# Kernel tuning notes

Hardware: AMD Instinct MI355X
Metric: run time of the kernel (lower is better)

Reference implementation:

```python
import jax, jax.numpy as jnp
import numpy as np

B, L, D = 4, 2048, 1024
H, DK, DV = 4, 256, 256
CHUNK = 32
MIN_FLOOR, MAX_FLOOR = 0.01, 0.1
EPS = 1e-5


def _l2norm(x):
    return x * jax.lax.rsqrt(jnp.sum(x * x, -1, keepdims=True) + 1e-6)


def _causal_dwconv(x, w):
    # x: [b, L, C], w: [C, k] -> depthwise causal 1d conv
    b, l, c = x.shape
    k = w.shape[-1]
    xt = jnp.transpose(x, (0, 2, 1))
    y = jax.lax.conv_general_dilated(xt, w[:, None, :], (1,), [(k - 1, 0)],
                                     dimension_numbers=('NCH', 'OIH', 'NCH'),
                                     feature_group_count=c)
    return jnp.transpose(y, (0, 2, 1))


def _delta_rule_chunkwise(q, k, v, beta, chunk=CHUNK):
    # q,k: [b,h,L,dk]; v: [b,h,L,dv]; beta: [b,h,L]; L % chunk == 0
    b, h, l, dk = q.shape
    dv = v.shape[-1]
    q = _l2norm(q)
    k = _l2norm(k)
    v = v * beta[..., None]
    kb = k * beta[..., None]
    n = l // chunk
    resh = lambda t: t.reshape(b, h, n, chunk, t.shape[-1])
    q, k, v, kb = resh(q), resh(k), resh(v), resh(kb)
    tri = jnp.triu(jnp.ones((chunk, chunk), bool))        # incl diag
    strict = jnp.triu(jnp.ones((chunk, chunk), bool), 1)  # excl diag
    att = jnp.where(tri, 0.0, -(kb @ jnp.swapaxes(k, -1, -2)))
    # UT transform: forward substitution building (I - lower)^{-1}
    for i in range(1, chunk):
        upd = jnp.einsum('bhnj,bhnjk->bhnk', att[..., i, :], att)
        att = att.at[..., i, :i].add(upd[..., :i])
    att = att + jnp.eye(chunk, dtype=att.dtype)
    u = att @ v
    w = att @ kb

    def step(S, xs):
        q_i, k_i, u_i, w_i = xs  # [b,h,chunk,d]
        local = jnp.where(strict, 0.0, q_i @ jnp.swapaxes(k_i, -1, -2))
        u_adj = u_i - w_i @ S
        o_i = q_i @ S + local @ u_adj
        return S + jnp.swapaxes(k_i, -1, -2) @ u_adj, o_i

    xs = tuple(jnp.moveaxis(t, 2, 0) for t in (q, k, u, w))
    S0 = jnp.zeros((b, h, dk, dv), q.dtype)
    S, o = jax.lax.scan(step, S0, xs)
    return jnp.moveaxis(o, 0, 2).reshape(b, h, l, dv), S


def _rmsnorm(x, w):
    return x * jax.lax.rsqrt(jnp.mean(x * x, -1, keepdims=True) + EPS) * w


def setup_inputs():
    key = jax.random.key(0)
    ks = jax.random.split(key, 16)
    s = 0.02
    return {
        'hidden_states': jax.random.normal(ks[0], (B, L, D), jnp.float32),
        'W_q': jax.random.normal(ks[1], (D, H * DK), jnp.float32) * s,
        'W_k': jax.random.normal(ks[2], (D, H * DK), jnp.float32) * s,
        'W_v': jax.random.normal(ks[3], (D, H * DV), jnp.float32) * s,
        'W_b': jax.random.normal(ks[4], (D, H), jnp.float32) * s,
        'conv_w_q': jax.random.normal(ks[5], (H * DK, 4), jnp.float32) * 0.3,
        'conv_w_k': jax.random.normal(ks[6], (H * DK, 4), jnp.float32) * 0.3,
        'conv_w_v': jax.random.normal(ks[7], (H * DV, 4), jnp.float32) * 0.3,
        'fir_short_w': jax.random.normal(ks[8], (H, DV, 3), jnp.float32) * 0.1,
        'fir_long_w': jax.random.normal(ks[9], (H, DV, 31), jnp.float32) * 0.1,
        'W_fuse1': jax.random.normal(ks[10], (D + 3 * H * DV, 2 * D), jnp.float32) * s,
        'b_fuse1': jnp.zeros((2 * D,), jnp.float32),
        'W_fuse2': jax.random.normal(ks[11], (2 * D, H * 4), jnp.float32) * s,
        'b_fuse2': jnp.zeros((H * 4,), jnp.float32).at[3::4].set(4.0),
        'others_log_tau': jnp.zeros((H,), jnp.float32),
        'norm_w': jnp.ones((DV,), jnp.float32),
        'W_o': jax.random.normal(ks[12], (H * DV, D), jnp.float32) * s,
    }


def reference(hidden_states, W_q, W_k, W_v, W_b, conv_w_q, conv_w_k, conv_w_v,
              fir_short_w, fir_long_w, W_fuse1, b_fuse1, W_fuse2, b_fuse2,
              others_log_tau, norm_w, W_o):
    b, l, d = hidden_states.shape
    # projections + mandatory short conv (silu activation)
    q = jax.nn.silu(_causal_dwconv(hidden_states @ W_q, conv_w_q))
    k = jax.nn.silu(_causal_dwconv(hidden_states @ W_k, conv_w_k))
    v = jax.nn.silu(_causal_dwconv(hidden_states @ W_v, conv_w_v))
    q = q.reshape(b, l, H, DK)
    k = k.reshape(b, l, H, DK)
    v = v.reshape(b, l, H, DV)
    beta = jax.nn.sigmoid(hidden_states @ W_b)  # [b,l,H]
    delta_out, _ = _delta_rule_chunkwise(
        jnp.transpose(q, (0, 2, 1, 3)), jnp.transpose(k, (0, 2, 1, 3)),
        jnp.transpose(v, (0, 2, 1, 3)), jnp.transpose(beta, (0, 2, 1)))
    delta_out = jnp.transpose(delta_out, (0, 2, 1, 3))  # [b,l,H,DV]
    # depthwise FIR paths on v
    vc = v.reshape(b, l, H * DV)
    fir_s = _causal_dwconv(vc, fir_short_w.reshape(H * DV, -1)).reshape(b, l, H, DV)
    fir_l = _causal_dwconv(vc, fir_long_w.reshape(H * DV, -1)).reshape(b, l, H, DV)
    # fusion gate MLP
    gate_in = jnp.concatenate([hidden_states, fir_s.reshape(b, l, -1),
                               fir_l.reshape(b, l, -1), delta_out.reshape(b, l, -1)], -1)
    hid = jax.nn.gelu(gate_in @ W_fuse1 + b_fuse1, approximate=False)
    logits = (hid @ W_fuse2 + b_fuse2).reshape(b, l, H, 4)
    p_raw = jax.nn.sigmoid(logits[..., 3])
    # token-adaptive context floor
    floor = MIN_FLOOR + (MAX_FLOOR - MIN_FLOOR) * (1.0 - p_raw)
    p_val = (1.0 - floor) * p_raw
    tau = jnp.exp(others_log_tau)  # per-head temperature
    others = jax.nn.softmax(logits[..., :3] / tau[None, None, :, None], -1)
    p_ctx = (1.0 - p_val)[..., None] * others
    o = (p_ctx[..., 0:1] * fir_s + p_ctx[..., 1:2] * fir_l +
         p_ctx[..., 2:3] * delta_out + p_val[..., None] * v)
    o = _rmsnorm(o, norm_w)
    return o.reshape(b, l, H * DV) @ W_o
```

## Files before the change

kernel.cpp:

```cpp
#include <hip/hip_runtime.h>
#include <hip/hip_bf16.h>

#define B_ 4
#define L_ 2048
#define D_ 1024
#define H_ 4
#define DK_ 256
#define DV_ 256
#define NCH 64
#define NTOK 8192

typedef __attribute__((ext_vector_type(8))) short bf16x8;
typedef __attribute__((ext_vector_type(4))) float f32x4;
typedef unsigned int u32;

__device__ __forceinline__ float bu2f(unsigned short u) {
    union { unsigned int i; float f; } x; x.i = ((unsigned int)u) << 16; return x.f;
}
__device__ __forceinline__ unsigned short f2bu(float f) {
    union { __hip_bfloat16 h; unsigned short u; } x; x.h = __float2bfloat16(f); return x.u;
}
#define MFMA16(a, b, c) __builtin_amdgcn_mfma_f32_16x16x32_bf16(a, b, c, 0, 0, 0)

__device__ __forceinline__ void gload16(const void* g, void* l) {
    __builtin_amdgcn_global_load_lds(
        (const __attribute__((address_space(1))) u32*)g,
        (__attribute__((address_space(3))) u32*)l, 16, 0, 0);
}

__global__ __launch_bounds__(256) void k_transpose(const float* __restrict__ in,
                                                   unsigned short* __restrict__ out,
                                                   int K, int N) {
    __shared__ float tile[32][33];
    int k0 = blockIdx.y * 32, n0 = blockIdx.x * 32;
    int tx = threadIdx.x & 31, ty = threadIdx.x >> 5;
#pragma unroll
    for (int r = 0; r < 4; ++r)
        tile[ty + 8 * r][tx] = in[(long)(k0 + ty + 8 * r) * N + n0 + tx];
    __syncthreads();
#pragma unroll
    for (int r = 0; r < 4; ++r)
        out[(long)(n0 + ty + 8 * r) * K + k0 + tx] = f2bu(tile[tx][ty + 8 * r]);
}

__global__ __launch_bounds__(256) void k_padT2(const float* __restrict__ W,
                                               unsigned short* __restrict__ out) {
    long idx = (long)blockIdx.x * 256 + threadIdx.x;
    int n = (int)(idx >> 11), k = (int)(idx & 2047);
    out[idx] = (n < 16) ? f2bu(W[k * 16 + n]) : (unsigned short)0;
}

__global__ __launch_bounds__(256) void k_cvt_beta(const float4* __restrict__ hs4,
                                                  const float* __restrict__ W_b,
                                                  unsigned short* __restrict__ gate_in,
                                                  float* __restrict__ beta) {
    int tok = blockIdx.x;
    int tid = threadIdx.x;
    float4 v = hs4[(long)tok * 256 + tid];
    ushort4 o;
    o.x = f2bu(v.x); o.y = f2bu(v.y); o.z = f2bu(v.z); o.w = f2bu(v.w);
    *reinterpret_cast<ushort4*>(&gate_in[(long)tok * 4096 + tid * 4]) = o;
    const float4* wb = reinterpret_cast<const float4*>(W_b);
    int c4 = tid * 4;
    float4 w0 = wb[c4], w1 = wb[c4 + 1], w2 = wb[c4 + 2], w3 = wb[c4 + 3];
    float s[4];
    s[0] = v.x * w0.x + v.y * w1.x + v.z * w2.x + v.w * w3.x;
    s[1] = v.x * w0.y + v.y * w1.y + v.z * w2.y + v.w * w3.y;
    s[2] = v.x * w0.z + v.y * w1.z + v.z * w2.z + v.w * w3.z;
    s[3] = v.x * w0.w + v.y * w1.w + v.z * w2.w + v.w * w3.w;
    int wave = tid >> 6, lane = tid & 63;
#pragma unroll
    for (int off = 32; off; off >>= 1)
#pragma unroll
        for (int h = 0; h < 4; ++h) s[h] += __shfl_down(s[h], off);
    __shared__ float red[4][4];
    if (lane == 0)
#pragma unroll
        for (int h = 0; h < 4; ++h) red[wave][h] = s[h];
    __syncthreads();
    if (tid < 4) {
        int h = tid;
        float tot = red[0][h] + red[1][h] + red[2][h] + red[3][h];
        int b = tok >> 11, l = tok & 2047;
        beta[((long)(b * H_ + h)) * L_ + l] = 1.f / (1.f + expf(-tot));
    }
}

template <int EPI>
__global__ __launch_bounds__(256, 3) void k_gemm(const unsigned short* __restrict__ A, int lda,
                                                 const unsigned short* __restrict__ BT, int ldb,
                                                 void* __restrict__ Cout, int ldc,
                                                 const float* __restrict__ bias,
                                                 int K, int gx) {
    __shared__ __align__(16) unsigned short As[128][64];
    __shared__ __align__(16) unsigned short Bs[128][64];
    const int tid = threadIdx.x;
    const int wave = tid >> 6, lane = tid & 63;
    const int wm = wave & 1, wn = wave >> 1;
    const int lr = lane & 15, lg = lane >> 4;
    const int nwg = gridDim.x;
    const int cpx = nwg >> 3;
    const int orig = blockIdx.x;
    const int wg = (orig & 7) * cpx + (orig >> 3);
    const int m0 = (wg / gx) * 128, n0 = (wg % gx) * 128;
    const int srow = wave * 32 + (lane >> 3);
    const int scol = (((lane & 7) ^ ((lane >> 3) & 7))) * 8;
    const unsigned short* Ap = &A[(long)(m0 + srow) * lda + scol];
    const unsigned short* Bp = &BT[(long)(n0 + srow) * ldb + scol];
    unsigned short* AsB = &As[wave * 32][0];
    unsigned short* BsB = &Bs[wave * 32][0];
    const unsigned short* AsF = &As[0][0];
    const unsigned short* BsF = &Bs[0][0];
    f32x4 acc[4][4] = {};
    for (int k0 = 0; k0 < K; k0 += 64) {
#pragma unroll
        for (int g = 0; g < 4; ++g) {
            gload16(Ap + (long)g * 8 * lda + k0, AsB + g * 8 * 64);
            gload16(Bp + (long)g * 8 * ldb + k0, BsB + g * 8 * 64);
        }
        __syncthreads();
#pragma unroll
        for (int ks = 0; ks < 2; ++ks) {
            bf16x8 af[4], bfr[4];
#pragma unroll
            for (int mt = 0; mt < 4; ++mt) {
                int r = wm * 64 + mt * 16 + lr;
                af[mt] = *reinterpret_cast<const bf16x8*>(
                    AsF + r * 64 + (((ks * 4 + lg) ^ (lr & 7)) * 8));
            }
#pragma unroll
            for (int nt = 0; nt < 4; ++nt) {
                int r = wn * 64 + nt * 16 + lr;
                bfr[nt] = *reinterpret_cast<const bf16x8*>(
                    BsF + r * 64 + (((ks * 4 + lg) ^ (lr & 7)) * 8));
            }
#pragma unroll
            for (int mt = 0; mt < 4; ++mt)
#pragma unroll
                for (int nt = 0; nt < 4; ++nt)
                    acc[mt][nt] = MFMA16(af[mt], bfr[nt], acc[mt][nt]);
        }
        __syncthreads();
    }
#pragma unroll
    for (int mt = 0; mt < 4; ++mt)
#pragma unroll
        for (int nt = 0; nt < 4; ++nt)
#pragma unroll
            for (int r = 0; r < 4; ++r) {
                int row = m0 + wm * 64 + mt * 16 + lg * 4 + r;
                int col = n0 + wn * 64 + nt * 16 + lr;
                float v = acc[mt][nt][r];
                if (EPI == 2) {
                    v += bias[col];
                    v = 0.5f * v * (1.f + erff(v * 0.70710678118f));
                }
                if (EPI == 0)
                    reinterpret_cast<float*>(Cout)[(long)row * ldc + col] = v;
                else
                    reinterpret_cast<unsigned short*>(Cout)[(long)row * ldc + col] = f2bu(v);
            }
}

__global__ __launch_bounds__(256) void k_fuse2(const unsigned short* __restrict__ hid,
                                               const unsigned short* __restrict__ Wf2Tp,
                                               float* __restrict__ logits4) {
    const int mt = blockIdx.x, kq = blockIdx.y;
    const int tid = threadIdx.x, wave = tid >> 6, lane = tid & 63;
    const int lr = lane & 15, lg = lane >> 4;
    const int m0 = mt * 128 + wave * 32;
    const int kb = kq * 512;
    const unsigned short* a0p = hid + (long)(m0 + lr) * 2048 + kb + lg * 8;
    const unsigned short* a1p = a0p + (long)16 * 2048;
    const unsigned short* bp = Wf2Tp + (long)lr * 2048 + kb + lg * 8;
    f32x4 acc0 = {0, 0, 0, 0}, acc1 = {0, 0, 0, 0};
#pragma unroll 4
    for (int kk = 0; kk < 16; ++kk) {
        bf16x8 a0 = *reinterpret_cast<const bf16x8*>(a0p + kk * 32);
        bf16x8 a1 = *reinterpret_cast<const bf16x8*>(a1p + kk * 32);
        bf16x8 b = *reinterpret_cast<const bf16x8*>(bp + kk * 32);
        acc0 = MFMA16(a0, b, acc0);
        acc1 = MFMA16(a1, b, acc1);
    }
    float* out = logits4 + (long)kq * NTOK * 16;
#pragma unroll
    for (int r = 0; r < 4; ++r) {
        out[(long)(m0 + lg * 4 + r) * 16 + lr] = acc0[r];
        out[(long)(m0 + 16 + lg * 4 + r) * 16 + lr] = acc1[r];
    }
}

__global__ __launch_bounds__(256) void k_conv_silu(const unsigned short* __restrict__ QKVp,
                                                   const float* __restrict__ cwq,
                                                   const float* __restrict__ cwk,
                                                   const float* __restrict__ cwv,
                                                   unsigned short* __restrict__ qn,
                                                   unsigned short* __restrict__ kn,
                                                   unsigned short* __restrict__ v_blc) {
    int tok = blockIdx.x;
    int b = tok >> 11, l = tok & 2047;
    int t = threadIdx.x;
    float y[12];
#pragma unroll
    for (int j = 0; j < 12; ++j) {
        int c = t + 256 * j;
        const float* cw = (j < 4) ? &cwq[c * 4] : (j < 8) ? &cwk[(c - 1024) * 4] : &cwv[(c - 2048) * 4];
        float s = 0.f;
#pragma unroll
        for (int jj = 0; jj < 4; ++jj) {
            int tl = l - 3 + jj;
            if (tl >= 0) s += bu2f(QKVp[((long)(b * L_ + tl)) * 3072 + c]) * cw[jj];
        }
        y[j] = s / (1.f + expf(-s));
    }
    float sq[8];
#pragma unroll
    for (int j = 0; j < 8; ++j) sq[j] = y[j] * y[j];
    int wave = t >> 6, lane = t & 63;
#pragma unroll
    for (int off = 32; off; off >>= 1)
#pragma unroll
        for (int j = 0; j < 8; ++j) sq[j] += __shfl_down(sq[j], off);
    __shared__ float red[4][8];
    if (lane == 0)
#pragma unroll
        for (int j = 0; j < 8; ++j) red[wave][j] = sq[j];
    __syncthreads();
    float tot[8];
#pragma unroll
    for (int j = 0; j < 8; ++j) tot[j] = red[0][j] + red[1][j] + red[2][j] + red[3][j];
#pragma unroll
    for (int h = 0; h < 4; ++h) {
        float sc = rsqrtf(tot[h] + 1e-6f);
        qn[((long)(b * H_ + h) * L_ + l) * 256 + t] = f2bu(y[h] * sc);
    }
#pragma unroll
    for (int h = 0; h < 4; ++h) {
        float sc = rsqrtf(tot[4 + h] + 1e-6f);
        kn[((long)(b * H_ + h) * L_ + l) * 256 + t] = f2bu(y[4 + h] * sc);
    }
#pragma unroll
    for (int h = 0; h < 4; ++h)
        v_blc[(long)tok * 1024 + h * 256 + t] = f2bu(y[8 + h]);
}

__global__ __launch_bounds__(256) void k_delta_chunk(const unsigned short* __restrict__ qn,
                                                     const unsigned short* __restrict__ kn,
                                                     const unsigned short* __restrict__ v_blc,
                                                     const float* __restrict__ beta,
                                                     unsigned short* __restrict__ u_buf,
                                                     unsigned short* __restrict__ w_buf,
                                                     unsigned short* __restrict__ local_buf,
                                                     unsigned short* __restrict__ kT_buf) {
    int bid = blockIdx.x;
    int n = bid & 63, bh = bid >> 6;
    int b = bh >> 2, h = bh & 3;
    int t0 = n * 32;
    __shared__ __align__(16) unsigned short k_s[32][264];
    __shared__ __align__(16) unsigned short vbT[256][40];
    __shared__ __align__(16) unsigned short kbT[256][40];
    __shared__ __align__(16) float att[32][33];
    __shared__ __align__(16) unsigned short att_b[32][40];
    __shared__ float bet[32];
    int tid = threadIdx.x, wave = tid >> 6, lane = tid & 63;
    int lr = lane & 15, lg = lane >> 4;

    {
        int row = tid >> 3;
        int cc = (tid & 7) * 32;
        float brow = beta[(long)bh * L_ + t0 + row];
        if ((tid & 7) == 0) bet[row] = brow;
        const uint4* kp = reinterpret_cast<const uint4*>(&kn[((long)bh * L_ + t0 + row) * 256 + cc]);
        const uint4* vp = reinterpret_cast<const uint4*>(&v_blc[((long)(b * L_ + t0 + row)) * 1024 + h * 256 + cc]);
        unsigned short kv[32], vv[32];
#pragma unroll
        for (int g = 0; g < 4; ++g) {
            uint4 x = kp[g];
            *reinterpret_cast<uint4*>(&kv[g * 8]) = x;
            *reinterpret_cast<uint4*>(&k_s[row][cc + g * 8]) = x;
            *reinterpret_cast<uint4*>(&vv[g * 8]) = vp[g];
        }
#pragma unroll
        for (int e = 0; e < 32; ++e) {
            kbT[cc + e][row] = f2bu(bu2f(kv[e]) * brow);
            vbT[cc + e][row] = f2bu(bu2f(vv[e]) * brow);
        }
    }
    __syncthreads();

    {
        unsigned short tmp[32];
#pragma unroll
        for (int t = 0; t < 32; ++t) tmp[t] = k_s[t][tid];
#pragma unroll
        for (int g = 0; g < 4; ++g)
            *reinterpret_cast<uint4*>(&kT_buf[((long)bid * 256 + tid) * 32 + g * 8]) =
                *reinterpret_cast<uint4*>(&tmp[g * 8]);
    }

    {
        int i0 = (wave & 1) * 16, j0 = (wave >> 1) * 16;
        f32x4 G = {0, 0, 0, 0}, S2 = {0, 0, 0, 0};
#pragma unroll
        for (int kk = 0; kk < 8; ++kk) {
            bf16x8 bk = *reinterpret_cast<const bf16x8*>(&k_s[j0 + lr][kk * 32 + lg * 8]);
            bf16x8 ak = *reinterpret_cast<const bf16x8*>(&k_s[i0 + lr][kk * 32 + lg * 8]);
            bf16x8 aq = *reinterpret_cast<const bf16x8*>(&qn[((long)bh * L_ + t0 + i0 + lr) * 256 + kk * 32 + lg * 8]);
            G = MFMA16(ak, bk, G);
            S2 = MFMA16(aq, bk, S2);
        }
#pragma unroll
        for (int r = 0; r < 4; ++r) {
            int i = i0 + lg * 4 + r, j = j0 + lr;
            att[i][j] = (j < i) ? -bet[i] * G[r] : 0.f;
            local_buf[(long)bid * 1024 + i * 32 + j] = f2bu((j <= i) ? S2[r] : 0.f);
        }
    }
    __syncthreads();

    for (int i = 1; i < 32; ++i) {
        float upd = 0.f;
        if (tid < i) {
            for (int j = tid + 1; j < i; ++j) upd += att[i][j] * att[j][tid];
        }
        __syncthreads();
        if (tid < i) att[i][tid] += upd;
        __syncthreads();
    }
    for (int e = tid; e < 1024; e += 256) {
        int i = e >> 5, j = e & 31;
        att_b[i][j] = f2bu(att[i][j] + ((i == j) ? 1.f : 0.f));
    }
    __syncthreads();

    {
        int mt = wave & 1;
        bf16x8 afr = *reinterpret_cast<const bf16x8*>(&att_b[mt * 16 + lr][lg * 8]);
        f32x4 z = {0, 0, 0, 0};
#pragma unroll
        for (int ntt = 0; ntt < 8; ++ntt) {
            int n0c = (wave >> 1) * 128 + ntt * 16;
            bf16x8 bu = *reinterpret_cast<const bf16x8*>(&vbT[n0c + lr][lg * 8]);
            bf16x8 bw = *reinterpret_cast<const bf16x8*>(&kbT[n0c + lr][lg * 8]);
            f32x4 ut = MFMA16(afr, bu, z);
            f32x4 wt = MFMA16(afr, bw, z);
#pragma unroll
            for (int r = 0; r < 4; ++r) {
                int t = mt * 16 + lg * 4 + r, c = n0c + lr;
                u_buf[((long)bid * 32 + t) * 256 + c] = f2bu(ut[r]);
                w_buf[((long)bid * 32 + t) * 256 + c] = f2bu(wt[r]);
            }
        }
    }
}

__global__ __launch_bounds__(256) void k_scan(const unsigned short* __restrict__ qn,
                                              const unsigned short* __restrict__ u_buf,
                                              const unsigned short* __restrict__ w_buf,
                                              const unsigned short* __restrict__ local_buf,
                                              const unsigned short* __restrict__ kT_buf,
                                              unsigned short* __restrict__ gate_in) {
    int bid = blockIdx.x;
    int bh = bid & 15, dvb = bid >> 4;
    int b = bh >> 2, h = bh & 3;
    int dc0 = dvb * 16;
    __shared__ __align__(16) unsigned short Tb[16][264];
    __shared__ __align__(16) unsigned short uaT[16][40];
    const int tid = threadIdx.x, wave = tid >> 6, lane = tid & 63;
    const int lr = lane & 15, lg = lane >> 4;
    const int wi = wave & 1;
    const bool isW = wave < 2;
    const int c0w = wave * 64;
    f32x4 Tacc[4] = {};
    for (int e = tid; e < 16 * 264; e += 256) (&Tb[0][0])[e] = 0;
    const unsigned short* q_bh = qn + (long)bh * L_ * 256;
    const unsigned short* u_bh = u_buf + (long)bh * 64 * 8192;
    const unsigned short* w_bh = w_buf + (long)bh * 64 * 8192;
    const unsigned short* l_bh = local_buf + (long)bh * 64 * 1024;
    const unsigned short* kT_bh = kT_buf + (long)bh * 64 * 8192;
    const unsigned short* wq_base = (isW ? w_bh : q_bh) + (16 * wi + lr) * 256;
    const unsigned short* u_base = u_bh + (16 * wi + lg * 4) * 256 + dc0 + lr;
    const unsigned short* l_base = l_bh + (16 * wi + lr) * 32 + lg * 8;
    const unsigned short* kT_base = kT_bh + (c0w + lr) * 32 + lg * 8;
    bf16x8 wqA[8], kB[4], lA = {};
    float uv[4];
    auto prefetch = [&](int n) {
        long o8 = (long)n * 8192;
#pragma unroll
        for (int kk = 0; kk < 8; ++kk)
            wqA[kk] = *reinterpret_cast<const bf16x8*>(wq_base + o8 + kk * 32 + lg * 8);
#pragma unroll
        for (int cc = 0; cc < 4; ++cc)
            kB[cc] = *reinterpret_cast<const bf16x8*>(kT_base + o8 + cc * 512);
        if (isW) {
#pragma unroll
            for (int r = 0; r < 4; ++r) uv[r] = bu2f(u_base[o8 + r * 256]);
        } else {
            lA = *reinterpret_cast<const bf16x8*>(l_base + (long)n * 1024);
        }
    };
    prefetch(0);
    __syncthreads();
    for (int n = 0; n < 64; ++n) {
        f32x4 P0 = {0, 0, 0, 0}, P1 = {0, 0, 0, 0};
#pragma unroll
        for (int kk = 0; kk < 8; kk += 2) {
            bf16x8 t0 = *reinterpret_cast<const bf16x8*>(&Tb[lr][kk * 32 + lg * 8]);
            bf16x8 t1 = *reinterpret_cast<const bf16x8*>(&Tb[lr][(kk + 1) * 32 + lg * 8]);
            P0 = MFMA16(wqA[kk], t0, P0);
            P1 = MFMA16(wqA[kk + 1], t1, P1);
        }
        f32x4 P;
#pragma unroll
        for (int r = 0; r < 4; ++r) P[r] = P0[r] + P1[r];
        if (isW) {
#pragma unroll
            for (int r = 0; r < 4; ++r)
                uaT[lr][16 * wi + lg * 4 + r] = f2bu(uv[r] - P[r]);
        }
        bf16x8 kBc[4];
#pragma unroll
        for (int cc = 0; cc < 4; ++cc) kBc[cc] = kB[cc];
        bf16x8 lAc = lA;
        if (n + 1 < 64) prefetch(n + 1);
        __syncthreads();
        bf16x8 uaA = *reinterpret_cast<const bf16x8*>(&uaT[lr][lg * 8]);
        if (!isW) {
            f32x4 O = MFMA16(lAc, uaA, P);
#pragma unroll
            for (int r = 0; r < 4; ++r) {
                long row = (long)b * L_ + n * 32 + 16 * wi + lg * 4 + r;
                gate_in[row * 4096 + 3072 + h * 256 + dc0 + lr] = f2bu(O[r]);
            }
        }
#pragma unroll
        for (int cc = 0; cc < 4; ++cc)
            Tacc[cc] = MFMA16(uaA, kBc[cc], Tacc[cc]);
#pragma unroll
        for (int cc = 0; cc < 4; ++cc)
#pragma unroll
            for (int r = 0; r < 4; ++r)
                Tb[lg * 4 + r][c0w + cc * 16 + lr] = f2bu(Tacc[cc][r]);
        __syncthreads();
    }
}

__global__ __launch_bounds__(256) void k_fir(const unsigned short* __restrict__ v_blc,
                                             const float* __restrict__ ws3,
                                             const float* __restrict__ wl31,
                                             unsigned short* __restrict__ gate_in) {
    __shared__ unsigned short xs[94][256];
    int b = blockIdx.y, tt = blockIdx.x * 64, c0 = blockIdx.z * 256;
    int tid = threadIdx.x;
    for (int r = 0; r < 94; ++r) {
        int t = tt - 30 + r;
        xs[r][tid] = (t >= 0) ? v_blc[((long)(b * L_ + t)) * 1024 + c0 + tid] : (unsigned short)0;
    }
    int c = c0 + tid;
    float wl[31], ws[3];
#pragma unroll
    for (int j = 0; j < 31; ++j) wl[j] = wl31[(long)c * 31 + j];
#pragma unroll
    for (int j = 0; j < 3; ++j) ws[j] = ws3[(long)c * 3 + j];
    __syncthreads();
    for (int t = 0; t < 64; ++t) {
        float accl = 0.f, accs = 0.f;
#pragma unroll
        for (int j = 0; j < 31; ++j) accl += bu2f(xs[t + j][tid]) * wl[j];
#pragma unroll
        for (int j = 0; j < 3; ++j) accs += bu2f(xs[t + 28 + j][tid]) * ws[j];
        long row = (long)b * L_ + tt + t;
        gate_in[row * 4096 + 1024 + c] = f2bu(accs);
        gate_in[row * 4096 + 2048 + c] = f2bu(accl);
    }
}

__global__ __launch_bounds__(256) void k_gate(const float* __restrict__ logits4,
                                              const float* __restrict__ b_fuse2,
                                              const float* __restrict__ log_tau,
                                              const float* __restrict__ norm_w,
                                              const unsigned short* __restrict__ gate_in,
                                              const unsigned short* __restrict__ v_blc,
                                              unsigned short* __restrict__ o_norm) {
    int tok = blockIdx.x;
    int tid = threadIdx.x;
    __shared__ float lg_s[16];
    __shared__ float red[4][4];
    if (tid < 16) {
        long o = (long)tok * 16 + tid;
        lg_s[tid] = logits4[o] + logits4[(long)NTOK * 16 + o] +
                    logits4[(long)2 * NTOK * 16 + o] + logits4[(long)3 * NTOK * 16 + o] +
                    b_fuse2[tid];
    }
    __syncthreads();
    float o[4];
#pragma unroll
    for (int h = 0; h < 4; ++h) {
        float l0 = lg_s[h * 4 + 0], l1 = lg_s[h * 4 + 1], l2 = lg_s[h * 4 + 2], l3 = lg_s[h * 4 + 3];
        float praw = 1.f / (1.f + expf(-l3));
        float fl_ = 0.01f + 0.09f * (1.f - praw);
        float pval = (1.f - fl_) * praw;
        float itau = expf(-log_tau[h]);
        float a0 = l0 * itau, a1 = l1 * itau, a2 = l2 * itau;
        float m = fmaxf(a0, fmaxf(a1, a2));
        float e0 = expf(a0 - m), e1 = expf(a1 - m), e2 = expf(a2 - m);
        float inv = (1.f - pval) / (e0 + e1 + e2);
        long base = (long)tok * 4096;
        float fs = bu2f(gate_in[base + 1024 + h * 256 + tid]);
        float flv = bu2f(gate_in[base + 2048 + h * 256 + tid]);
        float dd = bu2f(gate_in[base + 3072 + h * 256 + tid]);
        float vv = bu2f(v_blc[(long)tok * 1024 + h * 256 + tid]);
        o[h] = e0 * inv * fs + e1 * inv * flv + e2 * inv * dd + pval * vv;
    }
    int wave = tid >> 6, lane = tid & 63;
    float s[4];
#pragma unroll
    for (int h = 0; h < 4; ++h) s[h] = o[h] * o[h];
#pragma unroll
    for (int off = 32; off; off >>= 1)
#pragma unroll
        for (int h = 0; h < 4; ++h) s[h] += __shfl_down(s[h], off);
    if (lane == 0)
#pragma unroll
        for (int h = 0; h < 4; ++h) red[wave][h] = s[h];
    __syncthreads();
#pragma unroll
    for (int h = 0; h < 4; ++h) {
        float tot = red[0][h] + red[1][h] + red[2][h] + red[3][h];
        float sc = rsqrtf(tot * (1.f / 256.f) + 1e-5f);
        o_norm[(long)tok * 1024 + h * 256 + tid] = f2bu(o[h] * sc * norm_w[tid]);
    }
}

extern "C" void kernel_launch(void* const* d_in, const int* in_sizes, int n_in,
                              void* d_out, int out_size, void* d_ws, size_t ws_size,
                              hipStream_t stream) {
    const float* hs = (const float*)d_in[0];
    const float* W_q = (const float*)d_in[1];
    const float* W_k = (const float*)d_in[2];
    const float* W_v = (const float*)d_in[3];
    const float* W_b = (const float*)d_in[4];
    const float* cwq = (const float*)d_in[5];
    const float* cwk = (const float*)d_in[6];
    const float* cwv = (const float*)d_in[7];
    const float* fir_s_w = (const float*)d_in[8];
    const float* fir_l_w = (const float*)d_in[9];
    const float* W_f1 = (const float*)d_in[10];
    const float* b_f1 = (const float*)d_in[11];
    const float* W_f2 = (const float*)d_in[12];
    const float* b_f2 = (const float*)d_in[13];
    const float* log_tau = (const float*)d_in[14];
    const float* norm_w = (const float*)d_in[15];
    const float* W_o = (const float*)d_in[16];

    char* ws = (char*)d_ws;
    size_t off = 0;
    auto alloc = [&](size_t bytes) { size_t o = off; off += (bytes + 255) & ~(size_t)255; return o; };
    unsigned short* gate_in = (unsigned short*)(ws + alloc((size_t)NTOK * 4096 * 2));
    unsigned short* QKVp    = (unsigned short*)(ws + alloc((size_t)NTOK * 3072 * 2));
    unsigned short* WqkvT   = (unsigned short*)(ws + alloc((size_t)3072 * 1024 * 2));
    unsigned short* Wf1T    = (unsigned short*)(ws + alloc((size_t)2048 * 4096 * 2));
    unsigned short* WoT     = (unsigned short*)(ws + alloc((size_t)1024 * 1024 * 2));
    unsigned short* Wf2Tp   = (unsigned short*)(ws + alloc((size_t)128 * 2048 * 2));
    float*          beta    = (float*)(ws + alloc((size_t)16 * 2048 * 4));
    unsigned short* qn      = (unsigned short*)(ws + alloc((size_t)16 * 2048 * 256 * 2));
    unsigned short* kn      = (unsigned short*)(ws + alloc((size_t)16 * 2048 * 256 * 2));
    unsigned short* v_blc   = (unsigned short*)(ws + alloc((size_t)NTOK * 1024 * 2));
    unsigned short* u_buf   = (unsigned short*)(ws + alloc((size_t)16 * 64 * 8192 * 2));
    unsigned short* w_buf   = (unsigned short*)(ws + alloc((size_t)16 * 64 * 8192 * 2));
    unsigned short* locb    = (unsigned short*)(ws + alloc((size_t)16 * 64 * 1024 * 2));
    unsigned short* kT_buf  = (unsigned short*)(ws + alloc((size_t)16 * 64 * 8192 * 2));
    float*          logits4 = (float*)(ws + alloc((size_t)4 * NTOK * 16 * 4));
    unsigned short* o_norm  = (unsigned short*)(ws + alloc((size_t)NTOK * 1024 * 2));
    unsigned short* hid     = QKVp;

    k_transpose<<<dim3(32, 32), 256, 0, stream>>>(W_q, WqkvT, 1024, 1024);
    k_transpose<<<dim3(32, 32), 256, 0, stream>>>(W_k, WqkvT + (size_t)1024 * 1024, 1024, 1024);
    k_transpose<<<dim3(32, 32), 256, 0, stream>>>(W_v, WqkvT + (size_t)2048 * 1024, 1024, 1024);
    k_transpose<<<dim3(64, 128), 256, 0, stream>>>(W_f1, Wf1T, 4096, 2048);
    k_transpose<<<dim3(32, 32), 256, 0, stream>>>(W_o, WoT, 1024, 1024);
    k_padT2<<<1024, 256, 0, stream>>>(W_f2, Wf2Tp);
    k_cvt_beta<<<8192, 256, 0, stream>>>((const float4*)hs, W_b, gate_in, beta);
    k_gemm<1><<<24 * 64, 256, 0, stream>>>(gate_in, 4096, WqkvT, 1024, QKVp, 3072, nullptr,
                                           1024, 24);
    k_conv_silu<<<8192, 256, 0, stream>>>(QKVp, cwq, cwk, cwv, qn, kn, v_blc);
    k_delta_chunk<<<1024, 256, 0, stream>>>(qn, kn, v_blc, beta, u_buf, w_buf, locb, kT_buf);
    k_scan<<<256, 256, 0, stream>>>(qn, u_buf, w_buf, locb, kT_buf, gate_in);
    k_fir<<<dim3(32, 4, 4), 256, 0, stream>>>(v_blc, fir_s_w, fir_l_w, gate_in);
    k_gemm<2><<<16 * 64, 256, 0, stream>>>(gate_in, 4096, Wf1T, 4096, hid, 2048, b_f1,
                                           4096, 16);
    k_fuse2<<<dim3(64, 4), 256, 0, stream>>>(hid, Wf2Tp, logits4);
    k_gate<<<8192, 256, 0, stream>>>(logits4, b_f2, log_tau, norm_w, gate_in, v_blc, o_norm);
    k_gemm<0><<<8 * 64, 256, 0, stream>>>(o_norm, 1024, WoT, 1024, (float*)d_out, 1024, nullptr,
                                          1024, 8);
}
```

Baseline: 658.8 us.

## Single-wave UT forward substitution and double-buffered prefetch in delta-rule scan

The forward-substitution loop that builds the UT-transform matrix now runs on a single wavefront, using LDS waitcnt and sched barriers in place of two block-wide __syncthreads per row. This removes 62 block barriers. The sequential chunk scan now prefetches two chunks ahead with double-buffered register sets, and splits the W/Q loads from the K/local loads so they are issued at different points in the iteration. The P accumulation uses four independent MFMA chains instead of two. These changes add register pressure, and the wave-0-only path depends on LDS ordering within one wavefront being correct.

```diff
diff --git a/kernel.cpp b/kernel.cpp
--- a/kernel.cpp
+++ b/kernel.cpp
@@ -318,15 +318,20 @@
     }
     __syncthreads();
 
-    for (int i = 1; i < 32; ++i) {
-        float upd = 0.f;
-        if (tid < i) {
-            for (int j = tid + 1; j < i; ++j) upd += att[i][j] * att[j][tid];
-        }
-        __syncthreads();
-        if (tid < i) att[i][tid] += upd;
-        __syncthreads();
-    }
+    if (wave == 0) {
+        for (int i = 1; i < 32; ++i) {
+            float upd = 0.f;
+            if (lane < i) {
+                for (int j = lane + 1; j < i; ++j) upd += att[i][j] * att[j][lane];
+            }
+            asm volatile("s_waitcnt lgkmcnt(0)" ::: "memory");
+            __builtin_amdgcn_sched_barrier(0);
+            if (lane < i) att[i][lane] += upd;
+            asm volatile("s_waitcnt lgkmcnt(0)" ::: "memory");
+            __builtin_amdgcn_sched_barrier(0);
+        }
+    }
+    __syncthreads();
     for (int e = tid; e < 1024; e += 256) {
         int i = e >> 5, j = e & 31;
         att_b[i][j] = f2bu(att[i][j] + ((i == j) ? 1.f : 0.f));
@@ -382,67 +387,66 @@
     const unsigned short* u_base = u_bh + (16 * wi + lg * 4) * 256 + dc0 + lr;
     const unsigned short* l_base = l_bh + (16 * wi + lr) * 32 + lg * 8;
     const unsigned short* kT_base = kT_bh + (c0w + lr) * 32 + lg * 8;
-    bf16x8 wqA[8], kB[4], lA = {};
-    float uv[4];
-    auto prefetch = [&](int n) {
-        long o8 = (long)n * 8192;
-#pragma unroll
-        for (int kk = 0; kk < 8; ++kk)
-            wqA[kk] = *reinterpret_cast<const bf16x8*>(wq_base + o8 + kk * 32 + lg * 8);
-#pragma unroll
-        for (int cc = 0; cc < 4; ++cc)
-            kB[cc] = *reinterpret_cast<const bf16x8*>(kT_base + o8 + cc * 512);
-        if (isW) {
-#pragma unroll
-            for (int r = 0; r < 4; ++r) uv[r] = bu2f(u_base[o8 + r * 256]);
-        } else {
-            lA = *reinterpret_cast<const bf16x8*>(l_base + (long)n * 1024);
-        }
-    };
-    prefetch(0);
-    __syncthreads();
-    for (int n = 0; n < 64; ++n) {
-        f32x4 P0 = {0, 0, 0, 0}, P1 = {0, 0, 0, 0};
-#pragma unroll
-        for (int kk = 0; kk < 8; kk += 2) {
-            bf16x8 t0 = *reinterpret_cast<const bf16x8*>(&Tb[lr][kk * 32 + lg * 8]);
-            bf16x8 t1 = *reinterpret_cast<const bf16x8*>(&Tb[lr][(kk + 1) * 32 + lg * 8]);
-            P0 = MFMA16(wqA[kk], t0, P0);
-            P1 = MFMA16(wqA[kk + 1], t1, P1);
-        }
-        f32x4 P;
-#pragma unroll
-        for (int r = 0; r < 4; ++r) P[r] = P0[r] + P1[r];
-        if (isW) {
-#pragma unroll
-            for (int r = 0; r < 4; ++r)
-                uaT[lr][16 * wi + lg * 4 + r] = f2bu(uv[r] - P[r]);
-        }
-        bf16x8 kBc[4];
-#pragma unroll
-        for (int cc = 0; cc < 4; ++cc) kBc[cc] = kB[cc];
-        bf16x8 lAc = lA;
-        if (n + 1 < 64) prefetch(n + 1);
-        __syncthreads();
-        bf16x8 uaA = *reinterpret_cast<const bf16x8*>(&uaT[lr][lg * 8]);
-        if (!isW) {
-            f32x4 O = MFMA16(lAc, uaA, P);
-#pragma unroll
-            for (int r = 0; r < 4; ++r) {
-                long row = (long)b * L_ + n * 32 + 16 * wi + lg * 4 + r;
-                gate_in[row * 4096 + 3072 + h * 256 + dc0 + lr] = f2bu(O[r]);
-            }
-        }
-#pragma unroll
-        for (int cc = 0; cc < 4; ++cc)
-            Tacc[cc] = MFMA16(uaA, kBc[cc], Tacc[cc]);
-#pragma unroll
-        for (int cc = 0; cc < 4; ++cc)
-#pragma unroll
-            for (int r = 0; r < 4; ++r)
-                Tb[lg * 4 + r][c0w + cc * 16 + lr] = f2bu(Tacc[cc][r]);
-        __syncthreads();
-    }
+    bf16x8 wqA0[8], kB0[4], lA0 = {};
+    bf16x8 wqA1[8], kB1[4], lA1 = {};
+    float uv0[4] = {}, uv1[4] = {};
+
+#define PF_WQ(wqA_, uv_, n_) { long o8_ = (long)(n_) * 8192; \
+    _Pragma("unroll") for (int kk = 0; kk < 8; ++kk) \
+        wqA_[kk] = *reinterpret_cast<const bf16x8*>(wq_base + o8_ + kk * 32 + lg * 8); \
+    if (isW) { _Pragma("unroll") for (int r = 0; r < 4; ++r) uv_[r] = bu2f(u_base[o8_ + r * 256]); } }
+#define PF_KL(kB_, lA_, n_) { long o8_ = (long)(n_) * 8192; \
+    _Pragma("unroll") for (int cc = 0; cc < 4; ++cc) \
+        kB_[cc] = *reinterpret_cast<const bf16x8*>(kT_base + o8_ + cc * 512); \
+    if (!isW) lA_ = *reinterpret_cast<const bf16x8*>(l_base + (long)(n_) * 1024); }
+
+    PF_WQ(wqA0, uv0, 0) PF_KL(kB0, lA0, 0)
+    PF_WQ(wqA1, uv1, 1) PF_KL(kB1, lA1, 1)
+    __syncthreads();
+
+#define CHUNK_BODY(n_, wqA_, kB_, lA_, uv_) { \
+    f32x4 P0 = {0,0,0,0}, P1 = {0,0,0,0}, P2 = {0,0,0,0}, P3 = {0,0,0,0}; \
+    _Pragma("unroll") for (int kk = 0; kk < 2; ++kk) { \
+        bf16x8 t0 = *reinterpret_cast<const bf16x8*>(&Tb[lr][(kk * 4 + 0) * 32 + lg * 8]); \
+        bf16x8 t1 = *reinterpret_cast<const bf16x8*>(&Tb[lr][(kk * 4 + 1) * 32 + lg * 8]); \
+        bf16x8 t2 = *reinterpret_cast<const bf16x8*>(&Tb[lr][(kk * 4 + 2) * 32 + lg * 8]); \
+        bf16x8 t3 = *reinterpret_cast<const bf16x8*>(&Tb[lr][(kk * 4 + 3) * 32 + lg * 8]); \
+        P0 = MFMA16(wqA_[kk * 4 + 0], t0, P0); \
+        P1 = MFMA16(wqA_[kk * 4 + 1], t1, P1); \
+        P2 = MFMA16(wqA_[kk * 4 + 2], t2, P2); \
+        P3 = MFMA16(wqA_[kk * 4 + 3], t3, P3); \
+    } \
+    f32x4 P; \
+    _Pragma("unroll") for (int r = 0; r < 4; ++r) P[r] = (P0[r] + P1[r]) + (P2[r] + P3[r]); \
+    if (isW) { \
+        _Pragma("unroll") for (int r = 0; r < 4; ++r) \
+            uaT[lr][16 * wi + lg * 4 + r] = f2bu(uv_[r] - P[r]); \
+    } \
+    if ((n_) + 2 < 64) PF_WQ(wqA_, uv_, (n_) + 2) \
+    __syncthreads(); \
+    bf16x8 uaA = *reinterpret_cast<const bf16x8*>(&uaT[lr][lg * 8]); \
+    if (!isW) { \
+        f32x4 O = MFMA16(lA_, uaA, P); \
+        _Pragma("unroll") for (int r = 0; r < 4; ++r) { \
+            long row = (long)b * L_ + (n_) * 32 + 16 * wi + lg * 4 + r; \
+            gate_in[row * 4096 + 3072 + h * 256 + dc0 + lr] = f2bu(O[r]); \
+        } \
+    } \
+    _Pragma("unroll") for (int cc = 0; cc < 4; ++cc) \
+        Tacc[cc] = MFMA16(uaA, kB_[cc], Tacc[cc]); \
+    if ((n_) + 2 < 64) PF_KL(kB_, lA_, (n_) + 2) \
+    _Pragma("unroll") for (int cc = 0; cc < 4; ++cc) \
+        _Pragma("unroll") for (int r = 0; r < 4; ++r) \
+            Tb[lg * 4 + r][c0w + cc * 16 + lr] = f2bu(Tacc[cc][r]); \
+    __syncthreads(); }
+
+    for (int n = 0; n < 64; n += 2) {
+        CHUNK_BODY(n, wqA0, kB0, lA0, uv0)
+        CHUNK_BODY(n + 1, wqA1, kB1, lA1, uv1)
+    }
+#undef PF_WQ
+#undef PF_KL
+#undef CHUNK_BODY
 }
 
 __global__ __launch_bounds__(256) void k_fir(const unsigned short* __restrict__ v_blc,
```

Result: no change. 648.8 us (-1.5%).

## Double-buffer scan inputs via async global-to-LDS loads and single-wave UT solve

Applied to the files above, without the earlier changes.

The chunk scan kernel now stages W, Q, K^T, U and local tiles into swizzled double-buffered shared memory with direct global-to-LDS loads. Each next chunk is prefetched while the current one computes, replacing register prefetch, and barriers wait only on LDS counters. The UT forward substitution now runs in a single wave with waitcnt fences instead of block-wide barriers, removing 62 syncthreads per chunk. GEMM launch bounds are also raised to four blocks per SM, which may cause register spills.

```diff
diff --git a/kernel.cpp b/kernel.cpp
--- a/kernel.cpp
+++ b/kernel.cpp
@@ -27,6 +27,11 @@
         (const __attribute__((address_space(1))) u32*)g,
         (__attribute__((address_space(3))) u32*)l, 16, 0, 0);
 }
+
+#define RAWBAR() { asm volatile("s_waitcnt lgkmcnt(0)" ::: "memory"); \
+    __builtin_amdgcn_sched_barrier(0); \
+    __builtin_amdgcn_s_barrier(); \
+    __builtin_amdgcn_sched_barrier(0); }
 
 __global__ __launch_bounds__(256) void k_transpose(const float* __restrict__ in,
                                                    unsigned short* __restrict__ out,
@@ -87,7 +92,7 @@
 }
 
 template <int EPI>
-__global__ __launch_bounds__(256, 3) void k_gemm(const unsigned short* __restrict__ A, int lda,
+__global__ __launch_bounds__(256, 4) void k_gemm(const unsigned short* __restrict__ A, int lda,
                                                  const unsigned short* __restrict__ BT, int ldb,
                                                  void* __restrict__ Cout, int ldc,
                                                  const float* __restrict__ bias,
@@ -318,15 +323,20 @@
     }
     __syncthreads();
 
-    for (int i = 1; i < 32; ++i) {
-        float upd = 0.f;
-        if (tid < i) {
-            for (int j = tid + 1; j < i; ++j) upd += att[i][j] * att[j][tid];
-        }
-        __syncthreads();
-        if (tid < i) att[i][tid] += upd;
-        __syncthreads();
-    }
+    if (wave == 0) {
+        for (int i = 1; i < 32; ++i) {
+            float upd = 0.f;
+            if (lane < i) {
+                for (int j = lane + 1; j < i; ++j) upd += att[i][j] * att[j][lane];
+            }
+            asm volatile("s_waitcnt lgkmcnt(0)" ::: "memory");
+            __builtin_amdgcn_sched_barrier(0);
+            if (lane < i) att[i][lane] += upd;
+            asm volatile("s_waitcnt lgkmcnt(0)" ::: "memory");
+            __builtin_amdgcn_sched_barrier(0);
+        }
+    }
+    __syncthreads();
     for (int e = tid; e < 1024; e += 256) {
         int i = e >> 5, j = e & 31;
         att_b[i][j] = f2bu(att[i][j] + ((i == j) ? 1.f : 0.f));
@@ -354,16 +364,21 @@
     }
 }
 
-__global__ __launch_bounds__(256) void k_scan(const unsigned short* __restrict__ qn,
-                                              const unsigned short* __restrict__ u_buf,
-                                              const unsigned short* __restrict__ w_buf,
-                                              const unsigned short* __restrict__ local_buf,
-                                              const unsigned short* __restrict__ kT_buf,
-                                              unsigned short* __restrict__ gate_in) {
+__global__ __launch_bounds__(256, 1) void k_scan(const unsigned short* __restrict__ qn,
+                                                 const unsigned short* __restrict__ u_buf,
+                                                 const unsigned short* __restrict__ w_buf,
+                                                 const unsigned short* __restrict__ local_buf,
+                                                 const unsigned short* __restrict__ kT_buf,
+                                                 unsigned short* __restrict__ gate_in) {
     int bid = blockIdx.x;
     int bh = bid & 15, dvb = bid >> 4;
     int b = bh >> 2, h = bh & 3;
     int dc0 = dvb * 16;
+    __shared__ __align__(16) unsigned short Ws[2][32][256];
+    __shared__ __align__(16) unsigned short Qs[2][32][256];
+    __shared__ __align__(16) unsigned short KTs[2][256][32];
+    __shared__ __align__(16) unsigned short Us[2][32][16];
+    __shared__ __align__(16) unsigned short Ls[2][32][32];
     __shared__ __align__(16) unsigned short Tb[16][264];
     __shared__ __align__(16) unsigned short uaT[16][40];
     const int tid = threadIdx.x, wave = tid >> 6, lane = tid & 63;
@@ -378,55 +393,75 @@
     const unsigned short* w_bh = w_buf + (long)bh * 64 * 8192;
     const unsigned short* l_bh = local_buf + (long)bh * 64 * 1024;
     const unsigned short* kT_bh = kT_buf + (long)bh * 64 * 8192;
-    const unsigned short* wq_base = (isW ? w_bh : q_bh) + (16 * wi + lr) * 256;
-    const unsigned short* u_base = u_bh + (16 * wi + lg * 4) * 256 + dc0 + lr;
-    const unsigned short* l_base = l_bh + (16 * wi + lr) * 32 + lg * 8;
-    const unsigned short* kT_base = kT_bh + (c0w + lr) * 32 + lg * 8;
-    bf16x8 wqA[8], kB[4], lA = {};
-    float uv[4];
-    auto prefetch = [&](int n) {
-        long o8 = (long)n * 8192;
-#pragma unroll
-        for (int kk = 0; kk < 8; ++kk)
-            wqA[kk] = *reinterpret_cast<const bf16x8*>(wq_base + o8 + kk * 32 + lg * 8);
-#pragma unroll
-        for (int cc = 0; cc < 4; ++cc)
-            kB[cc] = *reinterpret_cast<const bf16x8*>(kT_base + o8 + cc * 512);
+
+    int wqrow[4], wqoff[4];
+#pragma unroll
+    for (int j = 0; j < 4; ++j) {
+        int i = wave * 4 + j;
+        int row = 2 * i + (lane >> 5);
+        wqrow[j] = 2 * i;
+        wqoff[j] = row * 256 + (((lane & 31) ^ (row & 7)) * 8);
+    }
+    int ktrow[4], ktoff[4];
+#pragma unroll
+    for (int j = 0; j < 4; ++j) {
+        int i = wave * 4 + j;
+        int row = i * 16 + (lane >> 2);
+        ktrow[j] = i * 16;
+        ktoff[j] = row * 32 + ((((lane & 3) ^ (row & 3)) ^ ((row >> 2) & 3)) * 8);
+    }
+    const int uoff = (lane >> 1) * 256 + dc0 + (lane & 1) * 8;
+    const int lrow = (wave - 1) * 16;
+    const int loff = (lrow + (lane >> 2)) * 32 + (lane & 3) * 8;
+
+#define STAGE(sl_, n_) { \
+    long o8_ = (long)(n_) * 8192; \
+    _Pragma("unroll") for (int j = 0; j < 4; ++j) { \
+        gload16(w_bh + o8_ + wqoff[j], &Ws[sl_][wqrow[j]][0]); \
+        gload16(q_bh + o8_ + wqoff[j], &Qs[sl_][wqrow[j]][0]); \
+        gload16(kT_bh + o8_ + ktoff[j], &KTs[sl_][ktrow[j]][0]); \
+    } \
+    if (wave == 0) gload16(u_bh + o8_ + uoff, &Us[sl_][0][0]); \
+    if (wave == 1 || wave == 2) gload16(l_bh + (long)(n_) * 1024 + loff, &Ls[sl_][lrow][0]); }
+
+    STAGE(0, 0)
+    asm volatile("s_waitcnt vmcnt(0)" ::: "memory");
+    __syncthreads();
+
+    for (int n = 0; n < 64; ++n) {
+        const int sl = n & 1;
+        if (n + 1 < 64) STAGE(sl ^ 1, n + 1)
+        const unsigned short* wq = isW ? &Ws[sl][0][0] : &Qs[sl][0][0];
+        f32x4 P0 = {0, 0, 0, 0}, P1 = {0, 0, 0, 0}, P2 = {0, 0, 0, 0}, P3 = {0, 0, 0, 0};
+#pragma unroll
+        for (int kk = 0; kk < 2; ++kk) {
+#pragma unroll
+            for (int q4 = 0; q4 < 4; ++q4) {
+                int kidx = kk * 4 + q4;
+                bf16x8 a = *reinterpret_cast<const bf16x8*>(
+                    wq + (16 * wi + lr) * 256 + (((kidx * 4 + lg) ^ (lr & 7)) * 8));
+                bf16x8 t = *reinterpret_cast<const bf16x8*>(&Tb[lr][kidx * 32 + lg * 8]);
+                if (q4 == 0) P0 = MFMA16(a, t, P0);
+                else if (q4 == 1) P1 = MFMA16(a, t, P1);
+                else if (q4 == 2) P2 = MFMA16(a, t, P2);
+                else P3 = MFMA16(a, t, P3);
+            }
+        }
+        f32x4 P;
+#pragma unroll
+        for (int r = 0; r < 4; ++r) P[r] = (P0[r] + P1[r]) + (P2[r] + P3[r]);
         if (isW) {
 #pragma unroll
-            for (int r = 0; r < 4; ++r) uv[r] = bu2f(u_base[o8 + r * 256]);
-        } else {
-            lA = *reinterpret_cast<const bf16x8*>(l_base + (long)n * 1024);
-        }
-    };
-    prefetch(0);
-    __syncthreads();
-    for (int n = 0; n < 64; ++n) {
-        f32x4 P0 = {0, 0, 0, 0}, P1 = {0, 0, 0, 0};
-#pragma unroll
-        for (int kk = 0; kk < 8; kk += 2) {
-            bf16x8 t0 = *reinterpret_cast<const bf16x8*>(&Tb[lr][kk * 32 + lg * 8]);
-            bf16x8 t1 = *reinterpret_cast<const bf16x8*>(&Tb[lr][(kk + 1) * 32 + lg * 8]);
-            P0 = MFMA16(wqA[kk], t0, P0);
-            P1 = MFMA16(wqA[kk + 1], t1, P1);
-        }
-        f32x4 P;
-#pragma unroll
-        for (int r = 0; r < 4; ++r) P[r] = P0[r] + P1[r];
-        if (isW) {
-#pragma unroll
-            for (int r = 0; r < 4; ++r)
-                uaT[lr][16 * wi + lg * 4 + r] = f2bu(uv[r] - P[r]);
-        }
-        bf16x8 kBc[4];
-#pragma unroll
-        for (int cc = 0; cc < 4; ++cc) kBc[cc] = kB[cc];
-        bf16x8 lAc = lA;
-        if (n + 1 < 64) prefetch(n + 1);
-        __syncthreads();
+            for (int r = 0; r < 4; ++r) {
+                float uv = bu2f(Us[sl][16 * wi + lg * 4 + r][lr]);
+                uaT[lr][16 * wi + lg * 4 + r] = f2bu(uv - P[r]);
+            }
+        }
+        RAWBAR()
         bf16x8 uaA = *reinterpret_cast<const bf16x8*>(&uaT[lr][lg * 8]);
         if (!isW) {
-            f32x4 O = MFMA16(lAc, uaA, P);
+            bf16x8 lA = *reinterpret_cast<const bf16x8*>(&Ls[sl][16 * wi + lr][lg * 8]);
+            f32x4 O = MFMA16(lA, uaA, P);
 #pragma unroll
             for (int r = 0; r < 4; ++r) {
                 long row = (long)b * L_ + n * 32 + 16 * wi + lg * 4 + r;
@@ -434,15 +469,21 @@
             }
         }
 #pragma unroll
-        for (int cc = 0; cc < 4; ++cc)
-            Tacc[cc] = MFMA16(uaA, kBc[cc], Tacc[cc]);
+        for (int cc = 0; cc < 4; ++cc) {
+            int rr = c0w + cc * 16 + lr;
+            bf16x8 kB = *reinterpret_cast<const bf16x8*>(
+                &KTs[sl][rr][(((lg ^ (rr & 3)) ^ ((rr >> 2) & 3)) * 8)]);
+            Tacc[cc] = MFMA16(uaA, kB, Tacc[cc]);
+        }
 #pragma unroll
         for (int cc = 0; cc < 4; ++cc)
 #pragma unroll
             for (int r = 0; r < 4; ++r)
                 Tb[lg * 4 + r][c0w + cc * 16 + lr] = f2bu(Tacc[cc][r]);
-        __syncthreads();
-    }
+        asm volatile("s_waitcnt vmcnt(0)" ::: "memory");
+        RAWBAR()
+    }
+#undef STAGE
 }
 
 __global__ __launch_bounds__(256) void k_fir(const unsigned short* __restrict__ v_blc,
```

New measurement: 637.1 us (median of 2 runs). 1.03x faster.
